# Performance work log

Hardware: AMD Instinct MI355X
Metric: run time of the kernel (lower is better)

The kernel has to match this reference:

```python
import jax, jax.numpy as jnp
import numpy as np
from jax import lax

# db5 (Daubechies-10) reconstruction lowpass filter, same values as pywt.Wavelet('db5').rec_lo
REC_LO = jnp.array([
    0.160102397974125,
    0.6038292697974729,
    0.7243085284385744,
    0.13842814590110342,
    -0.24229488706619015,
    -0.03224486958502952,
    0.07757149384006515,
    -0.006241490213011705,
    -0.012580751999015526,
    0.003335725285001549,
], dtype=jnp.float32)
DEC_LO = REC_LO[::-1]  # decomposition lowpass = reversed rec_lo
F = 10  # db5 filter length


def setup_inputs() -> dict:
    key = jax.random.key(0)
    x = jax.random.normal(key, (64, 128, 4096), dtype=jnp.float32)
    return {"x": x}


def reference(x) -> jnp.ndarray:
    # x: (B, C, L) -> flatten(1,2) -> (B, N) with N = C*L
    B, C, L = x.shape
    sig = x.reshape(B, 1, C * L)  # NCH layout, single channel

    # ---- DWT (db5, symmetric mode), lowpass branch only (cD is discarded upstream) ----
    # pywt equivalence: cA = np.convolve(pad(x, F-1, 'symmetric'), dec_lo, 'valid')[1::2]
    # np.convolve with dec_lo == correlation with rec_lo; offset-1 stride-2 downsampling
    ext = jnp.pad(sig, ((0, 0), (0, 0), (F - 1, F - 1)), mode="symmetric")
    k_dec = REC_LO.reshape(1, 1, F)
    cA = lax.conv_general_dilated(
        ext[:, :, 1:], k_dec,
        window_strides=(2,), padding=[(0, 0)],
        dimension_numbers=("NCH", "OIH", "NCH"),
    )  # (B, 1, (N+F-1)//2)

    # ---- IDWT from cA only: ya = pywt.idwt(cA, None, 'db5', 'smooth') ----
    # upsample by 2 (length 2*Nc-1), full-convolve with rec_lo, trim F-2 from each side
    # => transposed conv: lhs_dilation=2, correlation kernel = reversed rec_lo, pad (1,1)
    k_rec = DEC_LO.reshape(1, 1, F)
    ya = lax.conv_general_dilated(
        cA, k_rec,
        window_strides=(1,), padding=[(1, 1)], lhs_dilation=(2,),
        dimension_numbers=("NCH", "OIH", "NCH"),
    )  # (B, 1, 2*Nc - F + 2) -- matches torch .unsqueeze(1) output layout
    return ya
```

## Files before the change

### kernel.cpp

```cpp
#include <hip/hip_runtime.h>


#define L_SIG 524288
#define TILE 1024
#define SMEM_N (TILE + 32)

constexpr float RL[10] = {
    0.160102397974125f,   0.6038292697974729f,  0.7243085284385744f,
    0.13842814590110342f, -0.24229488706619015f, -0.03224486958502952f,
    0.07757149384006515f, -0.006241490213011705f, -0.012580751999015526f,
    0.003335725285001549f};

struct Coef { float we[18]; float wo[18]; };

constexpr Coef make_coef() {
    Coef c{};
    for (int d = 0; d < 18; ++d) {
        float se = 0.f, so = 0.f;
        for (int j = 0; j < 5; ++j) {
            int i = d - 2 * j;
            if (i >= 0 && i < 10) {
                se += RL[8 - 2 * j] * RL[i];
                so += RL[9 - 2 * j] * RL[i];
            }
        }
        c.we[d] = se;
        c.wo[d] = so;
    }
    return c;
}

constexpr Coef CF = make_coef();

__global__ __launch_bounds__(256)
void wavelet_fused_kernel(const float* __restrict__ x, float* __restrict__ out) {
    __shared__ float s[SMEM_N];

    const int batch = blockIdx.y;
    const int p0    = blockIdx.x * TILE;
    const float* xb = x   + (size_t)batch * L_SIG;
    float*       ob = out + (size_t)batch * L_SIG;

    const bool edge = (blockIdx.x == 0) || (blockIdx.x == gridDim.x - 1);

    if (edge) {
        for (int t = threadIdx.x; t < SMEM_N; t += 256) {
            int k  = p0 - 16 + t;
            int km = (k < 0) ? (-1 - k) : ((k >= L_SIG) ? (2 * L_SIG - 1 - k) : k);
            s[t] = xb[km];
        }
    } else {
        const float4* src = (const float4*)(xb + p0 - 16);
        float4* s4 = (float4*)s;
        int t = threadIdx.x;
        s4[t] = src[t];
        if (t < 8) s4[256 + t] = src[256 + t];
    }
    __syncthreads();

    const int q = threadIdx.x * 4;

    float v[20];
#pragma unroll
    for (int r = 0; r < 5; ++r) {
        float4 f = ((const float4*)(s + q + 8))[r];
        v[4 * r + 0] = f.x;
        v[4 * r + 1] = f.y;
        v[4 * r + 2] = f.z;
        v[4 * r + 3] = f.w;
    }

    float o0 = 0.f, o1 = 0.f, o2 = 0.f, o3 = 0.f;
#pragma unroll
    for (int d = 0; d < 18; ++d) {
        o0 += CF.we[d] * v[d];
        o1 += CF.wo[d] * v[d];
        o2 += CF.we[d] * v[d + 2];
        o3 += CF.wo[d] * v[d + 2];
    }

    float4 o = make_float4(o0, o1, o2, o3);
    *((float4*)(ob + p0 + q)) = o;
}

extern "C" void kernel_launch(void* const* d_in, const int* in_sizes, int n_in,
                              void* d_out, int out_size, void* d_ws, size_t ws_size,
                              hipStream_t stream) {
    const float* x = (const float*)d_in[0];
    float* out     = (float*)d_out;

    const int B = in_sizes[0] / L_SIG;
    dim3 grid(L_SIG / TILE, B);
    wavelet_fused_kernel<<<grid, 256, 0, stream>>>(x, out);
}
```

Before: 220.4 us.

## Drop shared-memory staging, load windows directly and compute two outputs with packed FMA

Each thread now reads its two 20-element input windows straight from global memory with float4 loads, no longer staging the tile in shared memory, so the block barrier goes away. Every block covers twice as many outputs, and each thread handles two positions 1024 apart, packing them into 2-wide vectors so the compiler can emit packed FP32 FMAs. The goal is less LDS traffic, sync overhead and instruction count. In exchange, overlapping windows are re-read from global memory and rely on cache hits, and the grid has half as many blocks.

```diff
diff --git a/kernel.cpp b/kernel.cpp
--- a/kernel.cpp
+++ b/kernel.cpp
@@ -1,9 +1,11 @@
 #include <hip/hip_runtime.h>
 
 
+typedef float f2 __attribute__((ext_vector_type(2)));
+
 #define L_SIG 524288
-#define TILE 1024
-#define SMEM_N (TILE + 32)
+#define SPAN  2048
+#define HALF  1024
 
 constexpr float RL[10] = {
     0.160102397974125f,   0.6038292697974729f,  0.7243085284385744f,
@@ -33,54 +35,63 @@
 constexpr Coef CF = make_coef();
 
 __global__ __launch_bounds__(256)
-void wavelet_fused_kernel(const float* __restrict__ x, float* __restrict__ out) {
-    __shared__ float s[SMEM_N];
-
+void wavelet_pk_kernel(const float* __restrict__ x, float* __restrict__ out) {
     const int batch = blockIdx.y;
-    const int p0    = blockIdx.x * TILE;
+    const int p0    = blockIdx.x * SPAN;
     const float* xb = x   + (size_t)batch * L_SIG;
     float*       ob = out + (size_t)batch * L_SIG;
 
+    const int t  = threadIdx.x;
+    const int qA = p0 + 4 * t;
+    const int qB = qA + HALF;
+
+    float wA[20], wB[20];
+
     const bool edge = (blockIdx.x == 0) || (blockIdx.x == gridDim.x - 1);
-
     if (edge) {
-        for (int t = threadIdx.x; t < SMEM_N; t += 256) {
-            int k  = p0 - 16 + t;
-            int km = (k < 0) ? (-1 - k) : ((k >= L_SIG) ? (2 * L_SIG - 1 - k) : k);
-            s[t] = xb[km];
+#pragma unroll
+        for (int i = 0; i < 20; ++i) {
+            int ka = qA + i - 8;
+            int kb = qB + i - 8;
+            ka = (ka < 0) ? (-1 - ka) : ((ka >= L_SIG) ? (2 * L_SIG - 1 - ka) : ka);
+            kb = (kb < 0) ? (-1 - kb) : ((kb >= L_SIG) ? (2 * L_SIG - 1 - kb) : kb);
+            wA[i] = xb[ka];
+            wB[i] = xb[kb];
         }
     } else {
-        const float4* src = (const float4*)(xb + p0 - 16);
-        float4* s4 = (float4*)s;
-        int t = threadIdx.x;
-        s4[t] = src[t];
-        if (t < 8) s4[256 + t] = src[256 + t];
-    }
-    __syncthreads();
-
-    const int q = threadIdx.x * 4;
-
-    float v[20];
+        const float4* a4 = (const float4*)(xb + qA - 8);
+        const float4* b4 = (const float4*)(xb + qB - 8);
 #pragma unroll
-    for (int r = 0; r < 5; ++r) {
-        float4 f = ((const float4*)(s + q + 8))[r];
-        v[4 * r + 0] = f.x;
-        v[4 * r + 1] = f.y;
-        v[4 * r + 2] = f.z;
-        v[4 * r + 3] = f.w;
+        for (int r = 0; r < 5; ++r) {
+            float4 fa = a4[r];
+            float4 fb = b4[r];
+            wA[4 * r + 0] = fa.x; wA[4 * r + 1] = fa.y;
+            wA[4 * r + 2] = fa.z; wA[4 * r + 3] = fa.w;
+            wB[4 * r + 0] = fb.x; wB[4 * r + 1] = fb.y;
+            wB[4 * r + 2] = fb.z; wB[4 * r + 3] = fb.w;
+        }
     }
 
-    float o0 = 0.f, o1 = 0.f, o2 = 0.f, o3 = 0.f;
+    f2 u[20];
+#pragma unroll
+    for (int i = 0; i < 20; ++i) {
+        f2 p; p[0] = wA[i]; p[1] = wB[i];
+        u[i] = p;
+    }
+
+    f2 e0 = 0.f, d1 = 0.f, e2 = 0.f, d3 = 0.f;
 #pragma unroll
     for (int d = 0; d < 18; ++d) {
-        o0 += CF.we[d] * v[d];
-        o1 += CF.wo[d] * v[d];
-        o2 += CF.we[d] * v[d + 2];
-        o3 += CF.wo[d] * v[d + 2];
+        e0 += CF.we[d] * u[d];
+        d1 += CF.wo[d] * u[d];
+        e2 += CF.we[d] * u[d + 2];
+        d3 += CF.wo[d] * u[d + 2];
     }
 
-    float4 o = make_float4(o0, o1, o2, o3);
-    *((float4*)(ob + p0 + q)) = o;
+    float4 oa = make_float4(e0[0], d1[0], e2[0], d3[0]);
+    float4 obv = make_float4(e0[1], d1[1], e2[1], d3[1]);
+    *((float4*)(ob + qA)) = oa;
+    *((float4*)(ob + qB)) = obv;
 }
 
 extern "C" void kernel_launch(void* const* d_in, const int* in_sizes, int n_in,
@@ -90,6 +101,6 @@
     float* out     = (float*)d_out;
 
     const int B = in_sizes[0] / L_SIG;
-    dim3 grid(L_SIG / TILE, B);
-    wavelet_fused_kernel<<<grid, 256, 0, stream>>>(x, out);
+    dim3 grid(L_SIG / SPAN, B);
+    wavelet_pk_kernel<<<grid, 256, 0, stream>>>(x, out);
 }
```

Measured after the change: 234.0 us. +6.2%, slower.
